# Optimization experiments

Hardware: AMD Instinct MI355X
Metric: run time of the kernel (lower is better)

The kernel has to match this reference:

```python
import jax, jax.numpy as jnp
import numpy as np

D, H, DK, L, F, V = 512, 16, 32, 16, 1024, 32768
C1, C2, CORE, LG, MD, B = 512, 256, 256, 64, 64, 16
T_IN = C1 + C2 + CORE      # 1024
T_TF = CORE + LG + MD      # 384


def _ln(x, g, b, eps=1e-5):
    mu = x.mean(-1, keepdims=True)
    var = ((x - mu) ** 2).mean(-1, keepdims=True)
    return (x - mu) * jax.lax.rsqrt(var + eps) * g + b


def _heads(x):  # [B,T,D] -> [B,H,T,DK]
    b, t, _ = x.shape
    return x.reshape(b, t, H, DK).transpose(0, 2, 1, 3)


def _summarizer(ids, sem, pos, inw, inb, outw, outb, tok, lng, lnb):
    b, t = ids.shape
    x = sem[ids] + pos[:t][None]                      # [B,T,D]
    wq, wk, wv = jnp.split(inw, 3, axis=0)
    bq, bk, bv = jnp.split(inb, 3, axis=0)
    q = _heads(jnp.broadcast_to(tok, (b, tok.shape[1], D)) @ wq.T + bq)
    k = _heads(x @ wk.T + bk)
    v = _heads(x @ wv.T + bv)
    s = jnp.einsum('bhqd,bhkd->bhqk', q, k) / jnp.sqrt(jnp.float32(DK))
    a = jax.nn.softmax(s, axis=-1)
    o = jnp.einsum('bhqk,bhkd->bhqd', a, v).transpose(0, 2, 1, 3).reshape(b, -1, D)
    return _ln(o @ outw.T + outb, lng, lnb)


def _forward(emb_sem, emb_pos,
             lg_sem, lg_pos, lg_inw, lg_inb, lg_outw, lg_outb, lg_tok, lg_lng, lg_lnb,
             md_sem, md_pos, md_inw, md_inb, md_outw, md_outb, md_tok, md_lng, md_lnb,
             qkv_w, qkv_b, wo_w, wo_b, ln1_g, ln1_b, ln2_g, ln2_b,
             ff1_w, ff1_b, ff2_w, ff2_b, hd_lng, hd_lnb, hd_w, hd_b,
             input_ids, target_ids):
    lg_ids = input_ids[:, -(C1 + C2 + CORE):-(C2 + CORE)]
    md_ids = input_ids[:, -(C2 + CORE):-CORE]
    core_ids = input_ids[:, -CORE:]
    tgt = target_ids[:, -CORE:]

    lg_emb = _summarizer(lg_ids, lg_sem, lg_pos, lg_inw, lg_inb, lg_outw, lg_outb, lg_tok, lg_lng, lg_lnb)
    md_emb = _summarizer(md_ids, md_sem, md_pos, md_inw, md_inb, md_outw, md_outb, md_tok, md_lng, md_lnb)
    x_core = emb_sem[core_ids] + emb_pos[:CORE][None]
    x = jnp.concatenate([lg_emb, md_emb, x_core], axis=1)   # [B, 384, D]

    mask = jnp.tril(jnp.ones((T_TF, T_TF), dtype=bool))

    def step(x, p):
        qw, qb, ow, ob, g1, b1, g2, b2, f1w, f1b, f2w, f2b = p
        h = _ln(x, g1, b1)
        qkv = h @ qw.T + qb
        q, k, v = (_heads(t) for t in jnp.split(qkv, 3, axis=-1))
        s = jnp.einsum('bhqd,bhkd->bhqk', q, k) / jnp.sqrt(jnp.float32(DK))
        s = jnp.where(mask, s, -jnp.inf)
        a = jax.nn.softmax(s, axis=-1)
        o = jnp.einsum('bhqk,bhkd->bhqd', a, v).transpose(0, 2, 1, 3).reshape(x.shape)
        x = x + o @ ow.T + ob
        h2 = _ln(x, g2, b2)
        ff = jax.nn.gelu(h2 @ f1w.T + f1b, approximate=False) @ f2w.T + f2b
        return x + ff, None

    x, _ = jax.lax.scan(step, x, (qkv_w, qkv_b, wo_w, wo_b, ln1_g, ln1_b,
                                  ln2_g, ln2_b, ff1_w, ff1_b, ff2_w, ff2_b))
    logits = (_ln(x, hd_lng, hd_lnb) @ hd_w.T + hd_b)[:, -CORE:, :]
    return logits, tgt


def setup_inputs() -> dict:
    key = jax.random.key(0)
    ks = jax.random.split(key, 24)
    def rn(k, shape, s=0.02):
        return jax.random.normal(k, shape, jnp.float32) * s
    z, o = jnp.zeros, jnp.ones
    return {
        'input_ids': jax.random.randint(ks[0], (B, T_IN), 0, V),
        'target_ids': jax.random.randint(ks[1], (B, T_IN), 0, V),
        'emb_sem': rn(ks[2], (V, D)), 'emb_pos': rn(ks[3], (CORE, D)),
        'lg_sem': rn(ks[4], (V, D)), 'lg_pos': rn(ks[5], (C1, D)),
        'lg_inw': rn(ks[6], (3 * D, D)), 'lg_inb': z(3 * D),
        'lg_outw': rn(ks[7], (D, D)), 'lg_outb': z(D),
        'lg_tok': rn(ks[8], (1, LG, D), 1.0), 'lg_lng': o(D), 'lg_lnb': z(D),
        'md_sem': rn(ks[9], (V, D)), 'md_pos': rn(ks[10], (C2, D)),
        'md_inw': rn(ks[11], (3 * D, D)), 'md_inb': z(3 * D),
        'md_outw': rn(ks[12], (D, D)), 'md_outb': z(D),
        'md_tok': rn(ks[13], (1, MD, D), 1.0), 'md_lng': o(D), 'md_lnb': z(D),
        'qkv_w': rn(ks[14], (L, 3 * D, D)), 'qkv_b': z((L, 3 * D)),
        'wo_w': rn(ks[15], (L, D, D)), 'wo_b': z((L, D)),
        'ln1_g': o((L, D)), 'ln1_b': z((L, D)), 'ln2_g': o((L, D)), 'ln2_b': z((L, D)),
        'ff1_w': rn(ks[16], (L, F, D)), 'ff1_b': z((L, F)),
        'ff2_w': rn(ks[17], (L, D, F)), 'ff2_b': z((L, D)),
        'hd_lng': o(D), 'hd_lnb': z(D), 'hd_w': rn(ks[18], (V, D)), 'hd_b': z(V),
    }


def reference(input_ids, target_ids, emb_sem, emb_pos,
              lg_sem, lg_pos, lg_inw, lg_inb, lg_outw, lg_outb, lg_tok, lg_lng, lg_lnb,
              md_sem, md_pos, md_inw, md_inb, md_outw, md_outb, md_tok, md_lng, md_lnb,
              qkv_w, qkv_b, wo_w, wo_b, ln1_g, ln1_b, ln2_g, ln2_b,
              ff1_w, ff1_b, ff2_w, ff2_b, hd_lng, hd_lnb, hd_w, hd_b):
    return _forward(emb_sem, emb_pos,
                    lg_sem, lg_pos, lg_inw, lg_inb, lg_outw, lg_outb, lg_tok, lg_lng, lg_lnb,
                    md_sem, md_pos, md_inw, md_inb, md_outw, md_outb, md_tok, md_lng, md_lnb,
                    qkv_w, qkv_b, wo_w, wo_b, ln1_g, ln1_b, ln2_g, ln2_b,
                    ff1_w, ff1_b, ff2_w, ff2_b, hd_lng, hd_lnb, hd_w, hd_b,
                    input_ids, target_ids)
```

## Files before the change

### kernel.cpp

```cpp
#include <hip/hip_runtime.h>
#include <hip/hip_bf16.h>
#include <math.h>

#define D 512
#define NHEAD 16
#define DK 32
#define NLAYER 16
#define FF 1024
#define VOC 32768
#define TTF 384
#define NCORE 256
#define NB 16

typedef __attribute__((ext_vector_type(8))) short bfrag;
typedef __attribute__((ext_vector_type(4))) float f32x4;

typedef __attribute__((address_space(3))) void lds_void;
typedef const __attribute__((address_space(1))) void gbl_void;
__device__ __forceinline__ void gload16(const void* g, void* l) {
    __builtin_amdgcn_global_load_lds((gbl_void*)g, (lds_void*)l, 16, 0, 0);
}

__device__ __forceinline__ float gelu_f(float v) {
    return 0.5f * v * (1.0f + erff(v * 0.70710678118654752f));
}

__device__ __forceinline__ void bf8_to_f32(uint4 u, float* v) {
    const __hip_bfloat16* t = reinterpret_cast<const __hip_bfloat16*>(&u);
    #pragma unroll
    for (int e = 0; e < 8; e++) v[e] = __bfloat162float(t[e]);
}
__device__ __forceinline__ uint4 f32_to_bf8(const float* v) {
    uint4 u; __hip_bfloat16* t = reinterpret_cast<__hip_bfloat16*>(&u);
    #pragma unroll
    for (int e = 0; e < 8; e++) t[e] = __float2bfloat16(v[e]);
    return u;
}

__global__ __launch_bounds__(256) void cvt_k(const float* __restrict__ in,
                                             __hip_bfloat16* __restrict__ out, int n)
{
    int i = (blockIdx.x * 256 + threadIdx.x) * 8;
    if (i >= n) return;
    float v[8];
    float4 a = *reinterpret_cast<const float4*>(in + i);
    float4 b = *reinterpret_cast<const float4*>(in + i + 4);
    v[0]=a.x; v[1]=a.y; v[2]=a.z; v[3]=a.w; v[4]=b.x; v[5]=b.y; v[6]=b.z; v[7]=b.w;
    *reinterpret_cast<uint4*>(out + i) = f32_to_bf8(v);
}

__global__ __launch_bounds__(256) void cvtpad_k(const float* __restrict__ in,
                                                __hip_bfloat16* __restrict__ out, int n, int ntot)
{
    int i = (blockIdx.x * 256 + threadIdx.x) * 8;
    if (i >= ntot) return;
    float v[8] = {0.f,0.f,0.f,0.f,0.f,0.f,0.f,0.f};
    if (i < n) {
        float4 a = *reinterpret_cast<const float4*>(in + i);
        float4 b = *reinterpret_cast<const float4*>(in + i + 4);
        v[0]=a.x; v[1]=a.y; v[2]=a.z; v[3]=a.w; v[4]=b.x; v[5]=b.y; v[6]=b.z; v[7]=b.w;
    }
    *reinterpret_cast<uint4*>(out + i) = f32_to_bf8(v);
}

__global__ __launch_bounds__(128) void embed_k(
    const int* __restrict__ ids, int id_stride, int id_off,
    const float* __restrict__ sem, const float* __restrict__ pos,
    __hip_bfloat16* __restrict__ out, int out_stride, int out_off)
{
    int t = blockIdx.x, b = blockIdx.y, tid = threadIdx.x;
    int id = ids[b * id_stride + id_off + t];
    const float4* s4 = reinterpret_cast<const float4*>(sem + (size_t)id * D);
    const float4* p4 = reinterpret_cast<const float4*>(pos + (size_t)t * D);
    size_t row = (size_t)(b * out_stride + out_off + t) * D;
    float4 a = s4[tid], p = p4[tid];
    __hip_bfloat16* o = out + row + tid * 4;
    o[0] = __float2bfloat16(a.x + p.x); o[1] = __float2bfloat16(a.y + p.y);
    o[2] = __float2bfloat16(a.z + p.z); o[3] = __float2bfloat16(a.w + p.w);
}

__global__ __launch_bounds__(256) void mgemm_k(
    const __hip_bfloat16* __restrict__ A, const __hip_bfloat16* __restrict__ W,
    const float* __restrict__ bias, void* __restrict__ C,
    int M, int N, int K, int flags, int order, int RT)
{
    __shared__ __align__(16) __hip_bfloat16 sA[2][8192];
    __shared__ __align__(16) __hip_bfloat16 sB[2][8192];
    int tid = threadIdx.x;
    int w = tid >> 6, lane = tid & 63;
    int wr = w >> 1, wc = w & 1;

    int nbx = gridDim.x, nby = gridDim.y;
    int nwg = nbx * nby;
    int bid0 = blockIdx.y * nbx + blockIdx.x;
    int bid = bid0;
    if (nwg >= 8) {
        int q = nwg >> 3, r = nwg & 7;
        int xcd = bid0 & 7, lb = bid0 >> 3;
        bid = (xcd < r ? xcd * (q + 1) : r * (q + 1) + (xcd - r) * q) + lb;
    }
    int bx, byg;
    if (order == 1) { bx = bid / nby; byg = bid - bx * nby; }
    else            { byg = bid / nbx; bx = bid - byg * nbx; }
    int col0 = bx * 128;

    int srow = lane >> 3;
    int scg  = (lane & 7) ^ srow;
    int cr = lane >> 4;
    int cc = lane & 15;

    auto stage = [&](int buf, int t, int k0) {
        int r0 = (byg * RT + t) * 128;
        #pragma unroll
        for (int r = 0; r < 4; r++) {
            int blk = r * 4 + w;
            const __hip_bfloat16* pa = A + (size_t)(r0 + blk * 8 + srow) * K + scg * 8 + k0;
            const __hip_bfloat16* pb = W + (size_t)(col0 + blk * 8 + srow) * K + scg * 8 + k0;
            gload16(pa, &sA[buf][blk * 512]);
            gload16(pb, &sB[buf][blk * 512]);
        }
    };

    int ksteps = K >> 6;
    int tsteps = RT * ksteps;

    stage(0, 0, 0);
    for (int t = 0; t < RT; t++) {
        int row0 = (byg * RT + t) * 128;

        f32x4 acc[4][4];
        #pragma unroll
        for (int m = 0; m < 4; m++)
            #pragma unroll
            for (int n = 0; n < 4; n++) acc[m][n] = (f32x4){0.f, 0.f, 0.f, 0.f};

        for (int kk = 0; kk < ksteps; kk++) {
            int s = t * ksteps + kk;
            int p = s & 1;
            if (s + 1 < tsteps) {
                int ns = s + 1;
                stage(p ^ 1, ns / ksteps, (ns % ksteps) << 6);
                asm volatile("s_waitcnt vmcnt(8)" ::: "memory");
            } else {
                asm volatile("s_waitcnt vmcnt(0)" ::: "memory");
            }
            __builtin_amdgcn_sched_barrier(0);
            __builtin_amdgcn_s_barrier();
            __builtin_amdgcn_sched_barrier(0);

            #pragma unroll
            for (int ks = 0; ks < 2; ks++) {
                bfrag af[4], bf[4];
                #pragma unroll
                for (int m = 0; m < 4; m++) {
                    int blk = wr * 8 + m * 2 + (cc >> 3);
                    int slot = (ks * 4 + cr) ^ (cc & 7);
                    af[m] = *reinterpret_cast<const bfrag*>(&sA[p][blk * 512 + (cc & 7) * 64 + slot * 8]);
                }
                #pragma unroll
                for (int n = 0; n < 4; n++) {
                    int blk = wc * 8 + n * 2 + (cc >> 3);
                    int slot = (ks * 4 + cr) ^ (cc & 7);
                    bf[n] = *reinterpret_cast<const bfrag*>(&sB[p][blk * 512 + (cc & 7) * 64 + slot * 8]);
                }
                #pragma unroll
                for (int m = 0; m < 4; m++)
                    #pragma unroll
                    for (int n = 0; n < 4; n++)
                        acc[m][n] = __builtin_amdgcn_mfma_f32_16x16x32_bf16(af[m], bf[n], acc[m][n], 0, 0, 0);
            }
            __builtin_amdgcn_sched_barrier(0);
            __builtin_amdgcn_s_barrier();
            __builtin_amdgcn_sched_barrier(0);
        }

        #pragma unroll
        for (int m = 0; m < 4; m++) {
            int rg = row0 + wr * 64 + m * 16 + cr * 4;
            #pragma unroll
            for (int n = 0; n < 4; n++) {
                int cg = col0 + wc * 64 + n * 16 + cc;
                float bs = bias[cg];
                #pragma unroll
                for (int j = 0; j < 4; j++) {
                    float v = acc[m][n][j] + bs;
                    size_t off = (size_t)(rg + j) * N + cg;
                    if (flags == 2)      ((__hip_bfloat16*)C)[off] = __float2bfloat16(gelu_f(v));
                    else if (flags == 3) ((__hip_bfloat16*)C)[off] = __float2bfloat16(v);
                    else                 ((float*)C)[off] = v;
                }
            }
        }
    }
}

template<int IB, int OB>
__global__ __launch_bounds__(256) void ln_k(
    const void* __restrict__ in, void* __restrict__ out,
    const float* __restrict__ g, const float* __restrict__ bt,
    int rpb, int in_stride, int in_off, int out_stride, int out_off)
{
    int r = blockIdx.x * 4 + (threadIdx.x >> 6);
    int b = r / rpb, t = r % rpb;
    size_t irow = (size_t)(b * in_stride + in_off + t) * D;
    size_t orow = (size_t)(b * out_stride + out_off + t) * D;
    int c0 = (threadIdx.x & 63) * 8;
    float v[8];
    if (IB) {
        bf8_to_f32(*reinterpret_cast<const uint4*>((const __hip_bfloat16*)in + irow + c0), v);
    } else {
        float4 a = *reinterpret_cast<const float4*>((const float*)in + irow + c0);
        float4 bq = *reinterpret_cast<const float4*>((const float*)in + irow + c0 + 4);
        v[0]=a.x; v[1]=a.y; v[2]=a.z; v[3]=a.w; v[4]=bq.x; v[5]=bq.y; v[6]=bq.z; v[7]=bq.w;
    }
    float s = 0.f;
    #pragma unroll
    for (int e = 0; e < 8; e++) s += v[e];
    #pragma unroll
    for (int off = 32; off; off >>= 1) s += __shfl_xor(s, off);
    float mu = s * (1.f / 512.f);
    float vs = 0.f;
    #pragma unroll
    for (int e = 0; e < 8; e++) { float d = v[e] - mu; vs += d * d; }
    #pragma unroll
    for (int off = 32; off; off >>= 1) vs += __shfl_xor(vs, off);
    float rstd = rsqrtf(vs * (1.f / 512.f) + 1e-5f);
    float y[8];
    #pragma unroll
    for (int e = 0; e < 8; e++) y[e] = (v[e] - mu) * rstd * g[c0 + e] + bt[c0 + e];
    if (OB) {
        *reinterpret_cast<uint4*>((__hip_bfloat16*)out + orow + c0) = f32_to_bf8(y);
    } else {
        *reinterpret_cast<float4*>((float*)out + orow + c0)     = make_float4(y[0], y[1], y[2], y[3]);
        *reinterpret_cast<float4*>((float*)out + orow + c0 + 4) = make_float4(y[4], y[5], y[6], y[7]);
    }
}

template<int WRITE_H>
__global__ __launch_bounds__(256) void res_ln_k(
    const __hip_bfloat16* __restrict__ delta, __hip_bfloat16* __restrict__ x,
    const float* __restrict__ g, const float* __restrict__ bt,
    __hip_bfloat16* __restrict__ h)
{
    int r = blockIdx.x * 4 + (threadIdx.x >> 6);
    int c0 = (threadIdx.x & 63) * 8;
    size_t row = (size_t)r * D + c0;
    float v[8], dv[8];
    bf8_to_f32(*reinterpret_cast<const uint4*>(x + row), v);
    bf8_to_f32(*reinterpret_cast<const uint4*>(delta + row), dv);
    #pragma unroll
    for (int e = 0; e < 8; e++) v[e] += dv[e];
    *reinterpret_cast<uint4*>(x + row) = f32_to_bf8(v);
    if (WRITE_H) {
        float s = 0.f;
        #pragma unroll
        for (int e = 0; e < 8; e++) s += v[e];
        #pragma unroll
        for (int off = 32; off; off >>= 1) s += __shfl_xor(s, off);
        float mu = s * (1.f / 512.f);
        float vs = 0.f;
        #pragma unroll
        for (int e = 0; e < 8; e++) { float d = v[e] - mu; vs += d * d; }
        #pragma unroll
        for (int off = 32; off; off >>= 1) vs += __shfl_xor(vs, off);
        float rstd = rsqrtf(vs * (1.f / 512.f) + 1e-5f);
        float y[8];
        #pragma unroll
        for (int e = 0; e < 8; e++) y[e] = (v[e] - mu) * rstd * g[c0 + e] + bt[c0 + e];
        *reinterpret_cast<uint4*>(h + row) = f32_to_bf8(y);
    }
}

__global__ __launch_bounds__(512) void fattn_k(
    const __hip_bfloat16* __restrict__ qkv, __hip_bfloat16* __restrict__ o)
{
    __shared__ __align__(16) __hip_bfloat16 Kl[24 * 512];
    __shared__ __align__(16) __hip_bfloat16 Vl[24 * 512];
    __shared__ __align__(16) __hip_bfloat16 Pl[8 * 512];
    int h = blockIdx.x, b = blockIdx.y;
    int tid = threadIdx.x, w = tid >> 6, l = tid & 63;
    const size_t base = (size_t)b * TTF * 1536 + h * DK;

    for (int it = 0; it < 3; it++) {
        int item = it * 512 + tid;
        int key = item >> 2, dg = item & 3;
        uint4 k4 = *reinterpret_cast<const uint4*>(qkv + base + (size_t)key * 1536 + 512 + dg * 8);
        *reinterpret_cast<uint4*>(&Kl[((key >> 4) * 64 + dg * 16 + (key & 15)) * 8]) = k4;
        uint4 v4 = *reinterpret_cast<const uint4*>(qkv + base + (size_t)key * 1536 + 1024 + dg * 8);
        const ushort* ve = reinterpret_cast<const ushort*>(&v4);
        #pragma unroll
        for (int e = 0; e < 8; e++) {
            int dk = dg * 8 + e;
            int f = (((key & 31) >> 3) << 4) | (dk & 15);
            int idx = (((key >> 5) << 1) + (dk >> 4)) * 512 + f * 8 + (key & 7);
            reinterpret_cast<ushort*>(Vl)[idx] = ve[e];
        }
    }
    __syncthreads();

    const float sc = 0.17677669529663687f;
    __hip_bfloat16* pw = Pl + w * 512;

    for (int iq = 0; iq < 3; iq++) {
        int qt = (iq == 0) ? w : (iq == 1 ? 15 - w : 16 + w);
        int q0 = qt * 16;
        bfrag qf = *reinterpret_cast<const bfrag*>(qkv + base + (size_t)(q0 + (l & 15)) * 1536 + (l >> 4) * 8);
        f32x4 oa0 = (f32x4){0.f, 0.f, 0.f, 0.f};
        f32x4 oa1 = (f32x4){0.f, 0.f, 0.f, 0.f};
        float mrun[4], lrun[4];
        #pragma unroll
        for (int jj = 0; jj < 4; jj++) { mrun[jj] = -3.0e38f; lrun[jj] = 0.f; }
        int ksmax = (q0 + 15) >> 5;

        for (int ks = 0; ks <= ksmax; ks++) {
            bfrag kf0 = *reinterpret_cast<const bfrag*>(&Kl[(ks * 2 + 0) * 512 + l * 8]);
            bfrag kf1 = *reinterpret_cast<const bfrag*>(&Kl[(ks * 2 + 1) * 512 + l * 8]);
            f32x4 z = (f32x4){0.f, 0.f, 0.f, 0.f};
            __builtin_amdgcn_s_setprio(1);
            f32x4 s0 = __builtin_amdgcn_mfma_f32_16x16x32_bf16(qf, kf0, z, 0, 0, 0);
            f32x4 s1 = __builtin_amdgcn_mfma_f32_16x16x32_bf16(qf, kf1, z, 0, 0, 0);
            __builtin_amdgcn_s_setprio(0);
            if (ks == ksmax) {
                #pragma unroll
                for (int jj = 0; jj < 4; jj++) {
                    int q = q0 + ((l >> 4) << 2) + jj;
                    if (ks * 32 + (l & 15) > q)      s0[jj] = -3.0e38f;
                    if (ks * 32 + 16 + (l & 15) > q) s1[jj] = -3.0e38f;
                }
            }
            float p0[4], p1[4], ps[4];
            #pragma unroll
            for (int jj = 0; jj < 4; jj++) {
                float sm = fmaxf(s0[jj], s1[jj]);
                #pragma unroll
                for (int off = 1; off <= 8; off <<= 1) sm = fmaxf(sm, __shfl_xor(sm, off));
                float mnew = fmaxf(mrun[jj], sm);
                float f = __expf((mrun[jj] - mnew) * sc);
                mrun[jj] = mnew;
                lrun[jj] *= f;
                oa0[jj] *= f; oa1[jj] *= f;
                p0[jj] = __expf((s0[jj] - mnew) * sc);
                p1[jj] = __expf((s1[jj] - mnew) * sc);
                ps[jj] = p0[jj] + p1[jj];
            }
            #pragma unroll
            for (int jj = 0; jj < 4; jj++) {
                float t = ps[jj];
                #pragma unroll
                for (int off = 1; off <= 8; off <<= 1) t += __shfl_xor(t, off);
                lrun[jj] += t;
            }
            #pragma unroll
            for (int jj = 0; jj < 4; jj++) {
                int ql = ((l >> 4) << 2) + jj;
                int kl0 = l & 15, kl1 = 16 + (l & 15);
                pw[((kl0 >> 3) * 16 + ql) * 8 + (kl0 & 7)] = __float2bfloat16(p0[jj]);
                pw[((kl1 >> 3) * 16 + ql) * 8 + (kl1 & 7)] = __float2bfloat16(p1[jj]);
            }
            bfrag pf  = *reinterpret_cast<const bfrag*>(&pw[l * 8]);
            bfrag vf0 = *reinterpret_cast<const bfrag*>(&Vl[(ks * 2 + 0) * 512 + l * 8]);
            bfrag vf1 = *reinterpret_cast<const bfrag*>(&Vl[(ks * 2 + 1) * 512 + l * 8]);
            __builtin_amdgcn_s_setprio(1);
            oa0 = __builtin_amdgcn_mfma_f32_16x16x32_bf16(pf, vf0, oa0, 0, 0, 0);
            oa1 = __builtin_amdgcn_mfma_f32_16x16x32_bf16(pf, vf1, oa1, 0, 0, 0);
            __builtin_amdgcn_s_setprio(0);
        }
        #pragma unroll
        for (int jj = 0; jj < 4; jj++) {
            float inv = 1.0f / lrun[jj];
            int q = q0 + ((l >> 4) << 2) + jj;
            size_t orow = ((size_t)b * TTF + q) * D + h * DK;
            o[orow + (l & 15)]      = __float2bfloat16(oa0[jj] * inv);
            o[orow + 16 + (l & 15)] = __float2bfloat16(oa1[jj] * inv);
        }
    }
}

template<int TLEN>
__global__ __launch_bounds__(256) void sattn_k(
    const __hip_bfloat16* __restrict__ q, const __hip_bfloat16* __restrict__ kv,
    __hip_bfloat16* __restrict__ o)
{
    __shared__ __align__(16) __hip_bfloat16 Kl[(TLEN / 16) * 512];
    __shared__ __align__(16) __hip_bfloat16 Vl[(TLEN / 16) * 512];
    __shared__ __align__(16) __hip_bfloat16 Pl[4 * 512];
    int h = blockIdx.x, b = blockIdx.y;
    int tid = threadIdx.x, w = tid >> 6, l = tid & 63;

    for (int it = 0; it < TLEN / 64; it++) {
        int item = it * 256 + tid;
        int key = item >> 2, dg = item & 3;
        const __hip_bfloat16* kr = kv + (size_t)(b * TLEN + key) * 1024 + h * DK + dg * 8;
        uint4 k4 = *reinterpret_cast<const uint4*>(kr);
        *reinterpret_cast<uint4*>(&Kl[((key >> 4) * 64 + dg * 16 + (key & 15)) * 8]) = k4;
        uint4 v4 = *reinterpret_cast<const uint4*>(kr + 512);
        const ushort* ve = reinterpret_cast<const ushort*>(&v4);
        #pragma unroll
        for (int e = 0; e < 8; e++) {
            int dk = dg * 8 + e;
            int f = (((key & 31) >> 3) << 4) | (dk & 15);
            int idx = (((key >> 5) << 1) + (dk >> 4)) * 512 + f * 8 + (key & 7);
            reinterpret_cast<ushort*>(Vl)[idx] = ve[e];
        }
    }
    __syncthreads();

    const float sc = 0.17677669529663687f;
    __hip_bfloat16* pw = Pl + w * 512;
    int q0 = w * 16;
    bfrag qf = *reinterpret_cast<const bfrag*>(q + (size_t)(q0 + (l & 15)) * D + h * DK + (l >> 4) * 8);
    f32x4 oa0 = (f32x4){0.f, 0.f, 0.f, 0.f};
    f32x4 oa1 = (f32x4){0.f, 0.f, 0.f, 0.f};
    float mrun[4], lrun[4];
    #pragma unroll
    for (int jj = 0; jj < 4; jj++) { mrun[jj] = -3.0e38f; lrun[jj] = 0.f; }

    for (int ks = 0; ks < TLEN / 32; ks++) {
        bfrag kf0 = *reinterpret_cast<const bfrag*>(&Kl[(ks * 2 + 0) * 512 + l * 8]);
        bfrag kf1 = *reinterpret_cast<const bfrag*>(&Kl[(ks * 2 + 1) * 512 + l * 8]);
        f32x4 z = (f32x4){0.f, 0.f, 0.f, 0.f};
        __builtin_amdgcn_s_setprio(1);
        f32x4 s0 = __builtin_amdgcn_mfma_f32_16x16x32_bf16(qf, kf0, z, 0, 0, 0);
        f32x4 s1 = __builtin_amdgcn_mfma_f32_16x16x32_bf16(qf, kf1, z, 0, 0, 0);
        __builtin_amdgcn_s_setprio(0);
        float p0[4], p1[4], ps[4];
        #pragma unroll
        for (int jj = 0; jj < 4; jj++) {
            float sm = fmaxf(s0[jj], s1[jj]);
            #pragma unroll
            for (int off = 1; off <= 8; off <<= 1) sm = fmaxf(sm, __shfl_xor(sm, off));
            float mnew = fmaxf(mrun[jj], sm);
            float f = __expf((mrun[jj] - mnew) * sc);
            mrun[jj] = mnew;
            lrun[jj] *= f;
            oa0[jj] *= f; oa1[jj] *= f;
            p0[jj] = __expf((s0[jj] - mnew) * sc);
            p1[jj] = __expf((s1[jj] - mnew) * sc);
            ps[jj] = p0[jj] + p1[jj];
        }
        #pragma unroll
        for (int jj = 0; jj < 4; jj++) {
            float t = ps[jj];
            #pragma unroll
            for (int off = 1; off <= 8; off <<= 1) t += __shfl_xor(t, off);
            lrun[jj] += t;
        }
        #pragma unroll
        for (int jj = 0; jj < 4; jj++) {
            int ql = ((l >> 4) << 2) + jj;
            int kl0 = l & 15, kl1 = 16 + (l & 15);
            pw[((kl0 >> 3) * 16 + ql) * 8 + (kl0 & 7)] = __float2bfloat16(p0[jj]);
            pw[((kl1 >> 3) * 16 + ql) * 8 + (kl1 & 7)] = __float2bfloat16(p1[jj]);
        }
        bfrag pf  = *reinterpret_cast<const bfrag*>(&pw[l * 8]);
        bfrag vf0 = *reinterpret_cast<const bfrag*>(&Vl[(ks * 2 + 0) * 512 + l * 8]);
        bfrag vf1 = *reinterpret_cast<const bfrag*>(&Vl[(ks * 2 + 1) * 512 + l * 8]);
        __builtin_amdgcn_s_setprio(1);
        oa0 = __builtin_amdgcn_mfma_f32_16x16x32_bf16(pf, vf0, oa0, 0, 0, 0);
        oa1 = __builtin_amdgcn_mfma_f32_16x16x32_bf16(pf, vf1, oa1, 0, 0, 0);
        __builtin_amdgcn_s_setprio(0);
    }
    #pragma unroll
    for (int jj = 0; jj < 4; jj++) {
        float inv = 1.0f / lrun[jj];
        int qi = q0 + ((l >> 4) << 2) + jj;
        size_t orow = ((size_t)b * 64 + qi) * D + h * DK;
        o[orow + (l & 15)]      = __float2bfloat16(oa0[jj] * inv);
        o[orow + 16 + (l & 15)] = __float2bfloat16(oa1[jj] * inv);
    }
}

__global__ __launch_bounds__(256) void tgt_k(const int* __restrict__ tids, float* __restrict__ out)
{
    int i = blockIdx.x * 256 + threadIdx.x;
    int b = i >> 8, c = i & 255;
    out[i] = (float)tids[b * 1024 + 768 + c];
}

extern "C" void kernel_launch(void* const* d_in, const int* in_sizes, int n_in,
                              void* d_out, int out_size, void* d_ws, size_t ws_size,
                              hipStream_t stream) {
    (void)in_sizes; (void)n_in; (void)out_size; (void)ws_size;
    const int*   input_ids  = (const int*)  d_in[0];
    const int*   target_ids = (const int*)  d_in[1];
    const float* emb_sem    = (const float*)d_in[2];
    const float* emb_pos    = (const float*)d_in[3];
    const float* lg_sem     = (const float*)d_in[4];
    const float* lg_pos     = (const float*)d_in[5];
    const float* lg_inw     = (const float*)d_in[6];
    const float* lg_inb     = (const float*)d_in[7];
    const float* lg_outw    = (const float*)d_in[8];
    const float* lg_outb    = (const float*)d_in[9];
    const float* lg_tok     = (const float*)d_in[10];
    const float* lg_lng     = (const float*)d_in[11];
    const float* lg_lnb     = (const float*)d_in[12];
    const float* md_sem     = (const float*)d_in[13];
    const float* md_pos     = (const float*)d_in[14];
    const float* md_inw     = (const float*)d_in[15];
    const float* md_inb     = (const float*)d_in[16];
    const float* md_outw    = (const float*)d_in[17];
    const float* md_outb    = (const float*)d_in[18];
    const float* md_tok     = (const float*)d_in[19];
    const float* md_lng     = (const float*)d_in[20];
    const float* md_lnb     = (const float*)d_in[21];
    const float* qkv_w      = (const float*)d_in[22];
    const float* qkv_b      = (const float*)d_in[23];
    const float* wo_w       = (const float*)d_in[24];
    const float* wo_b       = (const float*)d_in[25];
    const float* ln1_g      = (const float*)d_in[26];
    const float* ln1_b      = (const float*)d_in[27];
    const float* ln2_g      = (const float*)d_in[28];
    const float* ln2_b      = (const float*)d_in[29];
    const float* ff1_w      = (const float*)d_in[30];
    const float* ff1_b      = (const float*)d_in[31];
    const float* ff2_w      = (const float*)d_in[32];
    const float* ff2_b      = (const float*)d_in[33];
    const float* hd_lng     = (const float*)d_in[34];
    const float* hd_lnb     = (const float*)d_in[35];
    const float* hd_w       = (const float*)d_in[36];
    const float* hd_b       = (const float*)d_in[37];

    __hip_bfloat16* x_bf   = (__hip_bfloat16*)d_ws;
    __hip_bfloat16* h_bf   = x_bf   + 3145728;
    __hip_bfloat16* d_bf   = h_bf   + 3145728;
    __hip_bfloat16* a_bf   = d_bf   + 3145728;
    __hip_bfloat16* qkv_bf = a_bf   + 6291456;
    __hip_bfloat16* sumo_bf= qkv_bf + 9437184;
    __hip_bfloat16* w_qkv  = sumo_bf+ 524288;
    __hip_bfloat16* w_wo   = w_qkv  + 12582912;
    __hip_bfloat16* w_ff1  = w_wo   + 4194304;
    __hip_bfloat16* w_ff2  = w_ff1  + 8388608;
    __hip_bfloat16* w_hd   = w_ff2  + 8388608;
    __hip_bfloat16* w_lgin = w_hd   + 16777216;
    __hip_bfloat16* w_mdin = w_lgin + 786432;
    __hip_bfloat16* w_lgout= w_mdin + 786432;
    __hip_bfloat16* w_mdout= w_lgout+ 262144;
    __hip_bfloat16* tok_lg = w_mdout+ 262144;
    __hip_bfloat16* tok_md = tok_lg + 65536;
    __hip_bfloat16* q_bf   = tok_md + 65536;
    float* so2 = (float*)(q_bf + 65536);

    cvt_k<<<12582912 / 2048, 256, 0, stream>>>(qkv_w, w_qkv, 12582912);
    cvt_k<<< 4194304 / 2048, 256, 0, stream>>>(wo_w,  w_wo,   4194304);
    cvt_k<<< 8388608 / 2048, 256, 0, stream>>>(ff1_w, w_ff1,  8388608);
    cvt_k<<< 8388608 / 2048, 256, 0, stream>>>(ff2_w, w_ff2,  8388608);
    cvt_k<<<16777216 / 2048, 256, 0, stream>>>(hd_w,  w_hd,  16777216);
    cvt_k<<<  786432 / 2048, 256, 0, stream>>>(lg_inw, w_lgin, 786432);
    cvt_k<<<  786432 / 2048, 256, 0, stream>>>(md_inw, w_mdin, 786432);
    cvt_k<<<  262144 / 2048, 256, 0, stream>>>(lg_outw, w_lgout, 262144);
    cvt_k<<<  262144 / 2048, 256, 0, stream>>>(md_outw, w_mdout, 262144);
    cvtpad_k<<<32, 256, 0, stream>>>(lg_tok, tok_lg, 32768, 65536);
    cvtpad_k<<<32, 256, 0, stream>>>(md_tok, tok_md, 32768, 65536);

    embed_k<<<dim3(512, NB), 128, 0, stream>>>(input_ids, 1024, 0, lg_sem, lg_pos, a_bf, 512, 0);
    mgemm_k<<<dim3(8, 64), 256, 0, stream>>>(a_bf, w_lgin + 512 * 512, lg_inb + 512, qkv_bf, 8192, 1024, 512, 3, 0, 1);
    mgemm_k<<<dim3(4, 1), 256, 0, stream>>>(tok_lg, w_lgin, lg_inb, q_bf, 128, 512, 512, 3, 0, 1);
    sattn_k<512><<<dim3(NHEAD, NB), 256, 0, stream>>>(q_bf, qkv_bf, sumo_bf);
    mgemm_k<<<dim3(4, 8), 256, 0, stream>>>(sumo_bf, w_lgout, lg_outb, so2, 1024, 512, 512, 0, 0, 1);
    ln_k<0, 1><<<256, 256, 0, stream>>>(so2, x_bf, lg_lng, lg_lnb, 64, 64, 0, TTF, 0);

    embed_k<<<dim3(256, NB), 128, 0, stream>>>(input_ids, 1024, 512, md_sem, md_pos, a_bf, 256, 0);
    mgemm_k<<<dim3(8, 32), 256, 0, stream>>>(a_bf, w_mdin + 512 * 512, md_inb + 512, qkv_bf, 4096, 1024, 512, 3, 0, 1);
    mgemm_k<<<dim3(4, 1), 256, 0, stream>>>(tok_md, w_mdin, md_inb, q_bf, 128, 512, 512, 3, 0, 1);
    sattn_k<256><<<dim3(NHEAD, NB), 256, 0, stream>>>(q_bf, qkv_bf, sumo_bf);
    mgemm_k<<<dim3(4, 8), 256, 0, stream>>>(sumo_bf, w_mdout, md_outb, so2, 1024, 512, 512, 0, 0, 1);
    ln_k<0, 1><<<256, 256, 0, stream>>>(so2, x_bf, md_lng, md_lnb, 64, 64, 0, TTF, 64);

    embed_k<<<dim3(256, NB), 128, 0, stream>>>(input_ids, 1024, 768, emb_sem, emb_pos, x_bf, TTF, 128);

    ln_k<1, 1><<<1536, 256, 0, stream>>>(x_bf, h_bf, ln1_g, ln1_b, TTF, TTF, 0, TTF, 0);
    for (int l = 0; l < NLAYER; l++) {
        mgemm_k<<<dim3(12, 48), 256, 0, stream>>>(h_bf, w_qkv + (size_t)l * 1536 * 512, qkv_b + l * 1536, qkv_bf, 6144, 1536, 512, 3, 0, 1);
        fattn_k<<<dim3(NHEAD, NB), 512, 0, stream>>>(qkv_bf, a_bf);
        mgemm_k<<<dim3(4, 48), 256, 0, stream>>>(a_bf, w_wo + (size_t)l * 512 * 512, wo_b + l * D, d_bf, 6144, 512, 512, 3, 0, 1);
        res_ln_k<1><<<1536, 256, 0, stream>>>(d_bf, x_bf, ln2_g + l * D, ln2_b + l * D, h_bf);
        mgemm_k<<<dim3(8, 48), 256, 0, stream>>>(h_bf, w_ff1 + (size_t)l * 1024 * 512, ff1_b + l * FF, a_bf, 6144, 1024, 512, 2, 0, 1);
        mgemm_k<<<dim3(4, 48), 256, 0, stream>>>(a_bf, w_ff2 + (size_t)l * 512 * 1024, ff2_b + l * D, d_bf, 6144, 512, 1024, 3, 0, 1);
        if (l < NLAYER - 1) {
            res_ln_k<1><<<1536, 256, 0, stream>>>(d_bf, x_bf, ln1_g + (size_t)(l + 1) * D, ln1_b + (size_t)(l + 1) * D, h_bf);
        } else {
            res_ln_k<0><<<1536, 256, 0, stream>>>(d_bf, x_bf, hd_lng, hd_lnb, h_bf);
        }
    }

    ln_k<1, 1><<<1024, 256, 0, stream>>>(x_bf, h_bf, hd_lng, hd_lnb, NCORE, TTF, 128, NCORE, 0);
    float* logits = (float*)d_out;
    mgemm_k<<<dim3(256, 4), 256, 0, stream>>>(h_bf, w_hd, hd_b, logits, 4096, VOC, 512, 0, 1, 8);
    tgt_k<<<16, 256, 0, stream>>>(target_ids, logits + (size_t)NB * NCORE * VOC);
}
```

Baseline: 2.725 ms.

## Split causal attention across two blocks per head and fuse weight conversions

Attention now launches two blocks per (head, batch). One block handles query tiles 0-15 and loads only the first 256 keys. The other handles tiles 16-23 and loads all 384 keys. This doubles the grid to fill more CUs, at the cost of loading some keys twice. The eleven fp32-to-bf16 weight conversion launches are also merged into one kernel that branches on the index range, which removes launch overhead and relies on the destination buffers being contiguous.

```diff
diff --git a/kernel.cpp b/kernel.cpp
--- a/kernel.cpp
+++ b/kernel.cpp
@@ -37,27 +37,31 @@
     return u;
 }
 
-__global__ __launch_bounds__(256) void cvt_k(const float* __restrict__ in,
-                                             __hip_bfloat16* __restrict__ out, int n)
-{
-    int i = (blockIdx.x * 256 + threadIdx.x) * 8;
-    if (i >= n) return;
-    float v[8];
-    float4 a = *reinterpret_cast<const float4*>(in + i);
-    float4 b = *reinterpret_cast<const float4*>(in + i + 4);
-    v[0]=a.x; v[1]=a.y; v[2]=a.z; v[3]=a.w; v[4]=b.x; v[5]=b.y; v[6]=b.z; v[7]=b.w;
-    *reinterpret_cast<uint4*>(out + i) = f32_to_bf8(v);
-}
-
-__global__ __launch_bounds__(256) void cvtpad_k(const float* __restrict__ in,
-                                                __hip_bfloat16* __restrict__ out, int n, int ntot)
-{
-    int i = (blockIdx.x * 256 + threadIdx.x) * 8;
-    if (i >= ntot) return;
+__global__ __launch_bounds__(256) void cvtall_k(
+    const float* s0, const float* s1, const float* s2, const float* s3,
+    const float* s4, const float* s5, const float* s6, const float* s7,
+    const float* s8, const float* s9, const float* s10,
+    __hip_bfloat16* __restrict__ out)
+{
+    long long i = ((long long)blockIdx.x * 256 + threadIdx.x) * 8;
+    if (i >= 52559872LL) return;
+    const float* src; long long base; bool pad = false;
+    if      (i < 12582912LL) { src = s0;  base = 0LL; }
+    else if (i < 16777216LL) { src = s1;  base = 12582912LL; }
+    else if (i < 25165824LL) { src = s2;  base = 16777216LL; }
+    else if (i < 33554432LL) { src = s3;  base = 25165824LL; }
+    else if (i < 50331648LL) { src = s4;  base = 33554432LL; }
+    else if (i < 51118080LL) { src = s5;  base = 50331648LL; }
+    else if (i < 51904512LL) { src = s6;  base = 51118080LL; }
+    else if (i < 52166656LL) { src = s7;  base = 51904512LL; }
+    else if (i < 52428800LL) { src = s8;  base = 52166656LL; }
+    else if (i < 52494336LL) { src = s9;  base = 52428800LL; pad = true; }
+    else                     { src = s10; base = 52494336LL; pad = true; }
+    long long loc = i - base;
     float v[8] = {0.f,0.f,0.f,0.f,0.f,0.f,0.f,0.f};
-    if (i < n) {
-        float4 a = *reinterpret_cast<const float4*>(in + i);
-        float4 b = *reinterpret_cast<const float4*>(in + i + 4);
+    if (!pad || loc < 32768LL) {
+        float4 a = *reinterpret_cast<const float4*>(src + loc);
+        float4 b = *reinterpret_cast<const float4*>(src + loc + 4);
         v[0]=a.x; v[1]=a.y; v[2]=a.z; v[3]=a.w; v[4]=b.x; v[5]=b.y; v[6]=b.z; v[7]=b.w;
     }
     *reinterpret_cast<uint4*>(out + i) = f32_to_bf8(v);
@@ -277,11 +281,12 @@
     __shared__ __align__(16) __hip_bfloat16 Kl[24 * 512];
     __shared__ __align__(16) __hip_bfloat16 Vl[24 * 512];
     __shared__ __align__(16) __hip_bfloat16 Pl[8 * 512];
-    int h = blockIdx.x, b = blockIdx.y;
+    int h = blockIdx.x, b = blockIdx.y, part = blockIdx.z;
     int tid = threadIdx.x, w = tid >> 6, l = tid & 63;
     const size_t base = (size_t)b * TTF * 1536 + h * DK;
 
-    for (int it = 0; it < 3; it++) {
+    int niter = part ? 3 : 2;
+    for (int it = 0; it < niter; it++) {
         int item = it * 512 + tid;
         int key = item >> 2, dg = item & 3;
         uint4 k4 = *reinterpret_cast<const uint4*>(qkv + base + (size_t)key * 1536 + 512 + dg * 8);
@@ -301,8 +306,9 @@
     const float sc = 0.17677669529663687f;
     __hip_bfloat16* pw = Pl + w * 512;
 
-    for (int iq = 0; iq < 3; iq++) {
-        int qt = (iq == 0) ? w : (iq == 1 ? 15 - w : 16 + w);
+    int niq = part ? 1 : 2;
+    for (int iq = 0; iq < niq; iq++) {
+        int qt = part ? (16 + w) : (iq == 0 ? w : 15 - w);
         int q0 = qt * 16;
         bfrag qf = *reinterpret_cast<const bfrag*>(qkv + base + (size_t)(q0 + (l & 15)) * 1536 + (l >> 4) * 8);
         f32x4 oa0 = (f32x4){0.f, 0.f, 0.f, 0.f};
@@ -540,17 +546,9 @@
     __hip_bfloat16* q_bf   = tok_md + 65536;
     float* so2 = (float*)(q_bf + 65536);
 
-    cvt_k<<<12582912 / 2048, 256, 0, stream>>>(qkv_w, w_qkv, 12582912);
-    cvt_k<<< 4194304 / 2048, 256, 0, stream>>>(wo_w,  w_wo,   4194304);
-    cvt_k<<< 8388608 / 2048, 256, 0, stream>>>(ff1_w, w_ff1,  8388608);
-    cvt_k<<< 8388608 / 2048, 256, 0, stream>>>(ff2_w, w_ff2,  8388608);
-    cvt_k<<<16777216 / 2048, 256, 0, stream>>>(hd_w,  w_hd,  16777216);
-    cvt_k<<<  786432 / 2048, 256, 0, stream>>>(lg_inw, w_lgin, 786432);
-    cvt_k<<<  786432 / 2048, 256, 0, stream>>>(md_inw, w_mdin, 786432);
-    cvt_k<<<  262144 / 2048, 256, 0, stream>>>(lg_outw, w_lgout, 262144);
-    cvt_k<<<  262144 / 2048, 256, 0, stream>>>(md_outw, w_mdout, 262144);
-    cvtpad_k<<<32, 256, 0, stream>>>(lg_tok, tok_lg, 32768, 65536);
-    cvtpad_k<<<32, 256, 0, stream>>>(md_tok, tok_md, 32768, 65536);
+    cvtall_k<<<25664, 256, 0, stream>>>(qkv_w, wo_w, ff1_w, ff2_w, hd_w,
+                                        lg_inw, md_inw, lg_outw, md_outw,
+                                        lg_tok, md_tok, w_qkv);
 
     embed_k<<<dim3(512, NB), 128, 0, stream>>>(input_ids, 1024, 0, lg_sem, lg_pos, a_bf, 512, 0);
     mgemm_k<<<dim3(8, 64), 256, 0, stream>>>(a_bf, w_lgin + 512 * 512, lg_inb + 512, qkv_bf, 8192, 1024, 512, 3, 0, 1);
@@ -571,7 +569,7 @@
     ln_k<1, 1><<<1536, 256, 0, stream>>>(x_bf, h_bf, ln1_g, ln1_b, TTF, TTF, 0, TTF, 0);
     for (int l = 0; l < NLAYER; l++) {
         mgemm_k<<<dim3(12, 48), 256, 0, stream>>>(h_bf, w_qkv + (size_t)l * 1536 * 512, qkv_b + l * 1536, qkv_bf, 6144, 1536, 512, 3, 0, 1);
-        fattn_k<<<dim3(NHEAD, NB), 512, 0, stream>>>(qkv_bf, a_bf);
+        fattn_k<<<dim3(NHEAD, NB, 2), 512, 0, stream>>>(qkv_bf, a_bf);
         mgemm_k<<<dim3(4, 48), 256, 0, stream>>>(a_bf, w_wo + (size_t)l * 512 * 512, wo_b + l * D, d_bf, 6144, 512, 512, 3, 0, 1);
         res_ln_k<1><<<1536, 256, 0, stream>>>(d_bf, x_bf, ln2_g + l * D, ln2_b + l * D, h_bf);
         mgemm_k<<<dim3(8, 48), 256, 0, stream>>>(h_bf, w_ff1 + (size_t)l * 1024 * 512, ff1_b + l * FF, a_bf, 6144, 1024, 512, 2, 0, 1);
```

After: 2.679 ms. About the same (-1.7%).
